# Kernel optimization log

Measured on AMD Instinct MI355X. Metric: run time of the kernel, lower is better.

Reference implementation:

```python
import jax, jax.numpy as jnp
import numpy as np

B, TQ, T, E, H, D = 4, 2048, 2048, 2048, 16, 128
BLOCK = 4096
THETA = 10000.0


def _rope_tables():
    # LlamaRotaryEmbedding cos/sin cache of length BLOCK
    inv_freq = 1.0 / (THETA ** (jnp.arange(0, D, 2, dtype=jnp.float32) / D))
    t = jnp.arange(BLOCK, dtype=jnp.float32)
    freqs = jnp.einsum('i,j->ij', t, inv_freq)          # [BLOCK, D/2]
    emb = jnp.concatenate([freqs, freqs], axis=-1)      # [BLOCK, D]
    return jnp.cos(emb), jnp.sin(emb)


def _rotate_half(x):
    x1, x2 = jnp.split(x, 2, axis=-1)
    return jnp.concatenate([-x2, x1], axis=-1)


def setup_inputs() -> dict:
    key = jax.random.key(0)
    ks = jax.random.split(key, 9)
    s = 0.02
    x = jax.random.normal(ks[0], (B, TQ, E), dtype=jnp.float32)
    xall = jax.random.normal(ks[1], (B, T, E), dtype=jnp.float32)
    posx = jnp.sort(jax.random.randint(ks[2], (B, TQ), 0, BLOCK), axis=-1)
    posxall = jnp.sort(jax.random.randint(ks[3], (B, T), 0, BLOCK), axis=-1)
    mask = jax.random.bernoulli(ks[4], 0.15, (B, T))  # True = masked out
    Wq = jax.random.normal(ks[5], (E, H * D), dtype=jnp.float32) * s
    Wk = jax.random.normal(ks[6], (E, H * D), dtype=jnp.float32) * s
    Wv = jax.random.normal(ks[7], (E, H * D), dtype=jnp.float32) * s
    Wo = jax.random.normal(ks[8], (H * D, E), dtype=jnp.float32) * s
    return {"x": x, "xall": xall, "posx": posx, "posxall": posxall,
            "mask": mask, "Wq": Wq, "Wk": Wk, "Wv": Wv, "Wo": Wo}


def reference(x, xall, posx, posxall, mask, Wq, Wk, Wv, Wo):
    cos, sin = _rope_tables()
    # projections -> [B, H, T, D]
    q = (x @ Wq).reshape(B, TQ, H, D).transpose(0, 2, 1, 3)
    k = (xall @ Wk).reshape(B, T, H, D).transpose(0, 2, 1, 3)
    v = (xall @ Wv).reshape(B, T, H, D).transpose(0, 2, 1, 3)
    # gather-based RoPE with arbitrary per-token positions
    cosq = cos[posx][:, None]      # [B,1,TQ,D]
    sinq = sin[posx][:, None]
    cosk = cos[posxall][:, None]   # [B,1,T,D]
    sink = sin[posxall][:, None]
    q = q * cosq + _rotate_half(q) * sinq
    k = k * cosk + _rotate_half(k) * sink
    # explicit O(T^2) attention
    att = jnp.einsum('bhqd,bhkd->bhqk', q, k) * (1.0 / np.sqrt(D))
    att = jnp.where(mask[:, None, None, :], jnp.finfo(att.dtype).min, att)
    att = jax.nn.softmax(att, axis=-1)
    y = jnp.einsum('bhqk,bhkd->bhqd', att, v)
    y = y.transpose(0, 2, 1, 3).reshape(B, TQ, H * D)
    return y @ Wo
```

## Files before the change

kernel.cpp:

```cpp
#include <hip/hip_runtime.h>

typedef __bf16 bf16x8 __attribute__((ext_vector_type(8)));
typedef float f32x4 __attribute__((ext_vector_type(4)));

#define B_ 4
#define H_ 16
#define T_ 2048
#define E_ 2048
#define D_ 128

#define GLDS(g, l)                                                   \
  __builtin_amdgcn_global_load_lds(                                  \
      (const __attribute__((address_space(1))) void*)(g),            \
      (__attribute__((address_space(3))) void*)(l), 16, 0, 0)

__global__ __launch_bounds__(256) void cvt_f32_bf16(const float* __restrict__ in,
                                                    __bf16* __restrict__ out) {
  size_t i = ((size_t)blockIdx.x * 256 + threadIdx.x) * 8;
  float4 a = *(const float4*)(in + i);
  float4 b = *(const float4*)(in + i + 4);
  bf16x8 v;
  v[0] = (__bf16)a.x; v[1] = (__bf16)a.y; v[2] = (__bf16)a.z; v[3] = (__bf16)a.w;
  v[4] = (__bf16)b.x; v[5] = (__bf16)b.y; v[6] = (__bf16)b.z; v[7] = (__bf16)b.w;
  *(bf16x8*)(out + i) = v;
}

__global__ __launch_bounds__(256) void transpose_w(const float* __restrict__ W,
                                                   __bf16* __restrict__ Wt) {
  __shared__ float tile[32][33];
  int bx = blockIdx.x & 63, by = blockIdx.x >> 6;
  int tx = threadIdx.x & 31, ty = threadIdx.x >> 5;
#pragma unroll
  for (int i = 0; i < 4; i++)
    tile[ty + i * 8][tx] = W[(size_t)(by * 32 + ty + i * 8) * 2048 + bx * 32 + tx];
  __syncthreads();
#pragma unroll
  for (int i = 0; i < 4; i++)
    Wt[(size_t)(bx * 32 + ty + i * 8) * 2048 + by * 32 + tx] =
        (__bf16)tile[tx][ty + i * 8];
}

template <typename TOut>
__global__ __launch_bounds__(256, 2)
void gemm_bt(const __bf16* __restrict__ A, const __bf16* __restrict__ Bt,
             TOut* __restrict__ C, int N, int K) {
  __shared__ alignas(16) __bf16 As[128 * 32];
  __shared__ alignas(16) __bf16 Bs[128 * 32];
  const int ntiles = N >> 7;
  const int tm = blockIdx.x / ntiles, tn = blockIdx.x % ntiles;
  const int tid = threadIdx.x;
  const int wave = tid >> 6, lane = tid & 63, quad = lane >> 4, l16 = lane & 15;
  const int wrow = (wave >> 1) << 6, wcol = (wave & 1) << 6;

  const f32x4 z4 = {0.f, 0.f, 0.f, 0.f};
  f32x4 acc[4][4];
#pragma unroll
  for (int r = 0; r < 4; r++)
#pragma unroll
    for (int c = 0; c < 4; c++) acc[r][c] = z4;

  const int srow = wave * 16 + (lane >> 2);
  const int skc = ((lane & 3) ^ ((lane >> 2) & 3)) << 3;
  const __bf16* gA = A + ((size_t)tm * 128 + srow) * K + skc;
  const __bf16* gB = Bt + ((size_t)tn * 128 + srow) * K + skc;
  __bf16* lA = &As[wave * 512];
  __bf16* lB = &Bs[wave * 512];

  for (int k0 = 0; k0 < K; k0 += 32) {
    __syncthreads();
    GLDS(gA + k0, lA);
    GLDS(gA + (size_t)64 * K + k0, lA + 2048);
    GLDS(gB + k0, lB);
    GLDS(gB + (size_t)64 * K + k0, lB + 2048);
    __syncthreads();

    bf16x8 af[4], bfr[4];
#pragma unroll
    for (int r = 0; r < 4; r++) {
      int ar = wrow + r * 16 + l16;
      af[r] = *(const bf16x8*)&As[ar * 32 + ((quad ^ (ar & 3)) << 3)];
    }
#pragma unroll
    for (int c = 0; c < 4; c++) {
      int br = wcol + c * 16 + l16;
      bfr[c] = *(const bf16x8*)&Bs[br * 32 + ((quad ^ (br & 3)) << 3)];
    }
#pragma unroll
    for (int r = 0; r < 4; r++)
#pragma unroll
      for (int c = 0; c < 4; c++)
        acc[r][c] =
            __builtin_amdgcn_mfma_f32_16x16x32_bf16(af[r], bfr[c], acc[r][c], 0, 0, 0);
  }

  const size_t rbase = (size_t)tm * 128 + wrow + quad * 4;
  const int cbase = tn * 128 + wcol + l16;
#pragma unroll
  for (int r = 0; r < 4; r++)
#pragma unroll
    for (int c = 0; c < 4; c++)
#pragma unroll
      for (int e = 0; e < 4; e++)
        C[(rbase + r * 16 + e) * N + cbase + c * 16] = (TOut)acc[r][c][e];
}

__global__ __launch_bounds__(256) void rope_relayout(const __bf16* __restrict__ raw,
                                                     const int* __restrict__ pos,
                                                     __bf16* __restrict__ out,
                                                     float scale) {
  int row = blockIdx.x;
  int b = row >> 11, t = row & 2047;
  float p = (float)pos[row];
  for (int i = threadIdx.x; i < 1024; i += 256) {
    int h = i >> 6, d = i & 63;
    float inv = exp2f((float)d * -0.2076205059304601f);
    float ang = p * inv;
    float c = cosf(ang) * scale, s = sinf(ang) * scale;
    float q1 = (float)raw[(size_t)row * 2048 + h * 128 + d];
    float q2 = (float)raw[(size_t)row * 2048 + h * 128 + d + 64];
    size_t o = ((size_t)(b * 16 + h) * 2048 + t) * 128 + d;
    out[o] = (__bf16)(q1 * c - q2 * s);
    out[o + 64] = (__bf16)(q2 * c + q1 * s);
  }
}

__global__ __launch_bounds__(256) void vtrans(const __bf16* __restrict__ Vraw,
                                              __bf16* __restrict__ Vt) {
  __shared__ __bf16 tile[32][33];
  int dt = blockIdx.x & 3, tt = (blockIdx.x >> 2) & 63, bh = blockIdx.x >> 8;
  int b = bh >> 4, h = bh & 15;
  int tx = threadIdx.x & 31, ty = threadIdx.x >> 5;
#pragma unroll
  for (int i = 0; i < 4; i++) {
    int t = tt * 32 + ty + i * 8;
    tile[ty + i * 8][tx] = Vraw[(size_t)(b * T_ + t) * 2048 + h * 128 + dt * 32 + tx];
  }
  __syncthreads();
#pragma unroll
  for (int i = 0; i < 4; i++) {
    int d = dt * 32 + ty + i * 8;
    Vt[((size_t)bh * 128 + d) * T_ + tt * 32 + tx] = tile[tx][ty + i * 8];
  }
}

__global__ __launch_bounds__(256, 2)
void attn(const __bf16* __restrict__ Q, const __bf16* __restrict__ K,
          const __bf16* __restrict__ Vt, const int* __restrict__ mask,
          __bf16* __restrict__ Y) {
  __shared__ alignas(16) __bf16 Ks[64][136];
  __shared__ alignas(16) __bf16 Vs[128][72];
  __shared__ alignas(16) __bf16 Ps[4][16][72];

  const int qt = blockIdx.x & 31;
  const int bh = blockIdx.x >> 5;
  const int b = bh >> 4;
  const __bf16* Qb = Q + (size_t)bh * T_ * 128;
  const __bf16* Kb = K + (size_t)bh * T_ * 128;
  const __bf16* Vb = Vt + (size_t)bh * 128 * T_;
  const int* mb = mask + (size_t)b * T_;

  const int tid = threadIdx.x, wave = tid >> 6, lane = tid & 63;
  const int quad = lane >> 4, l16 = lane & 15;

  bf16x8 qf[4];
  {
    int qrow = qt * 64 + wave * 16 + l16;
#pragma unroll
    for (int kc = 0; kc < 4; kc++)
      qf[kc] = *(const bf16x8*)(Qb + (size_t)qrow * 128 + kc * 32 + quad * 8);
  }

  const f32x4 z4 = {0.f, 0.f, 0.f, 0.f};
  f32x4 o[8];
#pragma unroll
  for (int n = 0; n < 8; n++) o[n] = z4;
  float lacc[4] = {0.f, 0.f, 0.f, 0.f};

  for (int t0 = 0; t0 < T_; t0 += 64) {
    __syncthreads();
#pragma unroll
    for (int rr = 0; rr < 4; rr++) {
      int idx = rr * 256 + tid;
      *(uint4*)&Ks[idx >> 4][(idx & 15) << 3] =
          *(const uint4*)(Kb + (size_t)(t0 + (idx >> 4)) * 128 + ((idx & 15) << 3));
      *(uint4*)&Vs[idx >> 3][(idx & 7) << 3] =
          *(const uint4*)(Vb + (size_t)(idx >> 3) * T_ + t0 + ((idx & 7) << 3));
    }
    __syncthreads();

    f32x4 s[4];
#pragma unroll
    for (int c = 0; c < 4; c++) s[c] = z4;
#pragma unroll
    for (int c = 0; c < 4; c++)
#pragma unroll
      for (int kc = 0; kc < 4; kc++) {
        bf16x8 kf = *(const bf16x8*)&Ks[c * 16 + l16][kc * 32 + quad * 8];
        s[c] = __builtin_amdgcn_mfma_f32_16x16x32_bf16(qf[kc], kf, s[c], 0, 0, 0);
      }

    int mk[4];
#pragma unroll
    for (int c = 0; c < 4; c++) mk[c] = mb[t0 + c * 16 + l16];

    float p[4][4];
#pragma unroll
    for (int c = 0; c < 4; c++)
#pragma unroll
      for (int e = 0; e < 4; e++) {
        float v = __builtin_amdgcn_exp2f(s[c][e]);
        p[c][e] = mk[c] ? 0.f : v;
      }
#pragma unroll
    for (int e = 0; e < 4; e++)
      lacc[e] += (p[0][e] + p[1][e]) + (p[2][e] + p[3][e]);

#pragma unroll
    for (int c = 0; c < 4; c++)
#pragma unroll
      for (int e = 0; e < 4; e++)
        Ps[wave][quad * 4 + e][c * 16 + l16] = (__bf16)p[c][e];
    __builtin_amdgcn_wave_barrier();

#pragma unroll
    for (int kc = 0; kc < 2; kc++) {
      bf16x8 pf = *(const bf16x8*)&Ps[wave][l16][kc * 32 + quad * 8];
#pragma unroll
      for (int n = 0; n < 8; n++) {
        bf16x8 vf = *(const bf16x8*)&Vs[n * 16 + l16][kc * 32 + quad * 8];
        o[n] = __builtin_amdgcn_mfma_f32_16x16x32_bf16(pf, vf, o[n], 0, 0, 0);
      }
    }
    __builtin_amdgcn_wave_barrier();
  }

  const int hcol = (bh & 15) * 128;
  const size_t yrow0 = (size_t)b * T_ + qt * 64 + wave * 16 + quad * 4;
#pragma unroll
  for (int e = 0; e < 4; e++) {
    float l = lacc[e];
    l += __shfl_xor(l, 1, 16);
    l += __shfl_xor(l, 2, 16);
    l += __shfl_xor(l, 4, 16);
    l += __shfl_xor(l, 8, 16);
    float inv = 1.f / l;
#pragma unroll
    for (int n = 0; n < 8; n++)
      Y[(yrow0 + e) * 2048 + hcol + n * 16 + l16] = (__bf16)(o[n][e] * inv);
  }
}

extern "C" void kernel_launch(void* const* d_in, const int* in_sizes, int n_in,
                              void* d_out, int out_size, void* d_ws, size_t ws_size,
                              hipStream_t stream) {
  const float* x = (const float*)d_in[0];
  const float* xall = (const float*)d_in[1];
  const int* posx = (const int*)d_in[2];
  const int* posxall = (const int*)d_in[3];
  const int* mask = (const int*)d_in[4];
  const float* Wq = (const float*)d_in[5];
  const float* Wk = (const float*)d_in[6];
  const float* Wv = (const float*)d_in[7];
  const float* Wo = (const float*)d_in[8];
  float* out = (float*)d_out;

  const size_t MB = 1024ull * 1024ull;
  if (ws_size < 192 * MB) return;
  char* ws = (char*)d_ws;
  __bf16* WqT   = (__bf16*)(ws + 0 * MB);
  __bf16* WkT   = (__bf16*)(ws + 8 * MB);
  __bf16* WvT   = (__bf16*)(ws + 16 * MB);
  __bf16* WoT   = (__bf16*)(ws + 24 * MB);
  __bf16* xb    = (__bf16*)(ws + 32 * MB);
  __bf16* xallb = (__bf16*)(ws + 64 * MB);
  __bf16* Qraw  = (__bf16*)(ws + 96 * MB);
  __bf16* Kraw  = (__bf16*)(ws + 128 * MB);
  __bf16* Vraw  = (__bf16*)(ws + 160 * MB);
  __bf16* Qr    = xb;
  __bf16* Kr    = xallb;
  __bf16* Vtp   = Qraw;
  __bf16* Y     = Kraw;

  const float QSCALE = (float)(0.08838834764831843 * 1.4426950408889634);

  cvt_f32_bf16<<<8192, 256, 0, stream>>>(x, xb);
  cvt_f32_bf16<<<8192, 256, 0, stream>>>(xall, xallb);

  transpose_w<<<4096, 256, 0, stream>>>(Wq, WqT);
  transpose_w<<<4096, 256, 0, stream>>>(Wk, WkT);
  transpose_w<<<4096, 256, 0, stream>>>(Wv, WvT);
  transpose_w<<<4096, 256, 0, stream>>>(Wo, WoT);

  gemm_bt<__bf16><<<1024, 256, 0, stream>>>(xb, WqT, Qraw, 2048, 2048);
  gemm_bt<__bf16><<<1024, 256, 0, stream>>>(xallb, WkT, Kraw, 2048, 2048);
  gemm_bt<__bf16><<<1024, 256, 0, stream>>>(xallb, WvT, Vraw, 2048, 2048);

  rope_relayout<<<8192, 256, 0, stream>>>(Qraw, posx, Qr, QSCALE);
  rope_relayout<<<8192, 256, 0, stream>>>(Kraw, posxall, Kr, 1.0f);
  vtrans<<<16384, 256, 0, stream>>>(Vraw, Vtp);

  attn<<<2048, 256, 0, stream>>>(Qr, Kr, Vtp, mask, Y);

  gemm_bt<float><<<1024, 256, 0, stream>>>(Y, WoT, out, 2048, 2048);
}
```

Measured before the change: 820.7 us.

## Double query rows per attention wave to reuse K/V tiles; swizzle P buffer

Each attention wave now processes 32 query rows (two 16-row sub-tiles) instead of 16, so each block covers 128 queries and the grid halves. Every K/V tile loaded into shared memory and every fragment read from LDS is reused for twice as many MFMAs, cutting global and LDS traffic per unit of work. The P staging buffer drops its padding and uses an XOR swizzle to avoid bank conflicts. The GEMM launch bound also goes to 3 blocks per CU. Register pressure rises in attention, and the smaller grid may reduce occupancy or load balance.

```diff
diff --git a/kernel.cpp b/kernel.cpp
--- a/kernel.cpp
+++ b/kernel.cpp
@@ -41,7 +41,7 @@
 }
 
 template <typename TOut>
-__global__ __launch_bounds__(256, 2)
+__global__ __launch_bounds__(256, 3)
 void gemm_bt(const __bf16* __restrict__ A, const __bf16* __restrict__ Bt,
              TOut* __restrict__ C, int N, int K) {
   __shared__ alignas(16) __bf16 As[128 * 32];
@@ -149,10 +149,10 @@
           __bf16* __restrict__ Y) {
   __shared__ alignas(16) __bf16 Ks[64][136];
   __shared__ alignas(16) __bf16 Vs[128][72];
-  __shared__ alignas(16) __bf16 Ps[4][16][72];
-
-  const int qt = blockIdx.x & 31;
-  const int bh = blockIdx.x >> 5;
+  __shared__ alignas(16) __bf16 Ps[4][32][64];
+
+  const int qt = blockIdx.x & 15;
+  const int bh = blockIdx.x >> 4;
   const int b = bh >> 4;
   const __bf16* Qb = Q + (size_t)bh * T_ * 128;
   const __bf16* Kb = K + (size_t)bh * T_ * 128;
@@ -162,19 +162,23 @@
   const int tid = threadIdx.x, wave = tid >> 6, lane = tid & 63;
   const int quad = lane >> 4, l16 = lane & 15;
 
-  bf16x8 qf[4];
+  bf16x8 qf[2][4];
   {
-    int qrow = qt * 64 + wave * 16 + l16;
-#pragma unroll
-    for (int kc = 0; kc < 4; kc++)
-      qf[kc] = *(const bf16x8*)(Qb + (size_t)qrow * 128 + kc * 32 + quad * 8);
+    int qrow = qt * 128 + wave * 32 + l16;
+#pragma unroll
+    for (int sub = 0; sub < 2; sub++)
+#pragma unroll
+      for (int kc = 0; kc < 4; kc++)
+        qf[sub][kc] =
+            *(const bf16x8*)(Qb + (size_t)(qrow + sub * 16) * 128 + kc * 32 + quad * 8);
   }
 
   const f32x4 z4 = {0.f, 0.f, 0.f, 0.f};
-  f32x4 o[8];
-#pragma unroll
-  for (int n = 0; n < 8; n++) o[n] = z4;
-  float lacc[4] = {0.f, 0.f, 0.f, 0.f};
+  f32x4 o0[8], o1[8];
+#pragma unroll
+  for (int n = 0; n < 8; n++) { o0[n] = z4; o1[n] = z4; }
+  float lacc0[4] = {0.f, 0.f, 0.f, 0.f};
+  float lacc1[4] = {0.f, 0.f, 0.f, 0.f};
 
   for (int t0 = 0; t0 < T_; t0 += 64) {
     __syncthreads();
@@ -188,65 +192,69 @@
     }
     __syncthreads();
 
-    f32x4 s[4];
-#pragma unroll
-    for (int c = 0; c < 4; c++) s[c] = z4;
+    f32x4 s0[4], s1[4];
+#pragma unroll
+    for (int c = 0; c < 4; c++) { s0[c] = z4; s1[c] = z4; }
 #pragma unroll
     for (int c = 0; c < 4; c++)
 #pragma unroll
       for (int kc = 0; kc < 4; kc++) {
         bf16x8 kf = *(const bf16x8*)&Ks[c * 16 + l16][kc * 32 + quad * 8];
-        s[c] = __builtin_amdgcn_mfma_f32_16x16x32_bf16(qf[kc], kf, s[c], 0, 0, 0);
+        s0[c] = __builtin_amdgcn_mfma_f32_16x16x32_bf16(qf[0][kc], kf, s0[c], 0, 0, 0);
+        s1[c] = __builtin_amdgcn_mfma_f32_16x16x32_bf16(qf[1][kc], kf, s1[c], 0, 0, 0);
       }
 
     int mk[4];
 #pragma unroll
     for (int c = 0; c < 4; c++) mk[c] = mb[t0 + c * 16 + l16];
 
-    float p[4][4];
-#pragma unroll
-    for (int c = 0; c < 4; c++)
+#pragma unroll
+    for (int c = 0; c < 4; c++) {
+      int pcol = (c * 16 + l16) ^ (quad << 4);
 #pragma unroll
       for (int e = 0; e < 4; e++) {
-        float v = __builtin_amdgcn_exp2f(s[c][e]);
-        p[c][e] = mk[c] ? 0.f : v;
+        float v0 = __builtin_amdgcn_exp2f(s0[c][e]);
+        float v1 = __builtin_amdgcn_exp2f(s1[c][e]);
+        v0 = mk[c] ? 0.f : v0;
+        v1 = mk[c] ? 0.f : v1;
+        lacc0[e] += v0;
+        lacc1[e] += v1;
+        Ps[wave][quad * 4 + e][pcol] = (__bf16)v0;
+        Ps[wave][16 + quad * 4 + e][pcol] = (__bf16)v1;
       }
-#pragma unroll
-    for (int e = 0; e < 4; e++)
-      lacc[e] += (p[0][e] + p[1][e]) + (p[2][e] + p[3][e]);
-
-#pragma unroll
-    for (int c = 0; c < 4; c++)
-#pragma unroll
-      for (int e = 0; e < 4; e++)
-        Ps[wave][quad * 4 + e][c * 16 + l16] = (__bf16)p[c][e];
+    }
     __builtin_amdgcn_wave_barrier();
 
+    const int g4 = (l16 >> 2) << 4;
 #pragma unroll
     for (int kc = 0; kc < 2; kc++) {
-      bf16x8 pf = *(const bf16x8*)&Ps[wave][l16][kc * 32 + quad * 8];
+      bf16x8 pf0 = *(const bf16x8*)&Ps[wave][l16][(kc * 32 + quad * 8) ^ g4];
+      bf16x8 pf1 = *(const bf16x8*)&Ps[wave][16 + l16][(kc * 32 + quad * 8) ^ g4];
 #pragma unroll
       for (int n = 0; n < 8; n++) {
         bf16x8 vf = *(const bf16x8*)&Vs[n * 16 + l16][kc * 32 + quad * 8];
-        o[n] = __builtin_amdgcn_mfma_f32_16x16x32_bf16(pf, vf, o[n], 0, 0, 0);
+        o0[n] = __builtin_amdgcn_mfma_f32_16x16x32_bf16(pf0, vf, o0[n], 0, 0, 0);
+        o1[n] = __builtin_amdgcn_mfma_f32_16x16x32_bf16(pf1, vf, o1[n], 0, 0, 0);
       }
     }
     __builtin_amdgcn_wave_barrier();
   }
 
   const int hcol = (bh & 15) * 128;
-  const size_t yrow0 = (size_t)b * T_ + qt * 64 + wave * 16 + quad * 4;
+  const size_t yrow0 = (size_t)b * T_ + qt * 128 + wave * 32 + quad * 4;
 #pragma unroll
   for (int e = 0; e < 4; e++) {
-    float l = lacc[e];
-    l += __shfl_xor(l, 1, 16);
-    l += __shfl_xor(l, 2, 16);
-    l += __shfl_xor(l, 4, 16);
-    l += __shfl_xor(l, 8, 16);
-    float inv = 1.f / l;
-#pragma unroll
-    for (int n = 0; n < 8; n++)
-      Y[(yrow0 + e) * 2048 + hcol + n * 16 + l16] = (__bf16)(o[n][e] * inv);
+    float l0 = lacc0[e], l1 = lacc1[e];
+    l0 += __shfl_xor(l0, 1, 16); l1 += __shfl_xor(l1, 1, 16);
+    l0 += __shfl_xor(l0, 2, 16); l1 += __shfl_xor(l1, 2, 16);
+    l0 += __shfl_xor(l0, 4, 16); l1 += __shfl_xor(l1, 4, 16);
+    l0 += __shfl_xor(l0, 8, 16); l1 += __shfl_xor(l1, 8, 16);
+    float i0 = 1.f / l0, i1 = 1.f / l1;
+#pragma unroll
+    for (int n = 0; n < 8; n++) {
+      Y[(yrow0 + e) * 2048 + hcol + n * 16 + l16] = (__bf16)(o0[n][e] * i0);
+      Y[(yrow0 + 16 + e) * 2048 + hcol + n * 16 + l16] = (__bf16)(o1[n][e] * i1);
+    }
   }
 }
 
@@ -299,7 +307,7 @@
   rope_relayout<<<8192, 256, 0, stream>>>(Kraw, posxall, Kr, 1.0f);
   vtrans<<<16384, 256, 0, stream>>>(Vraw, Vtp);
 
-  attn<<<2048, 256, 0, stream>>>(Qr, Kr, Vtp, mask, Y);
+  attn<<<1024, 256, 0, stream>>>(Qr, Kr, Vtp, mask, Y);
 
   gemm_bt<float><<<1024, 256, 0, stream>>>(Y, WoT, out, 2048, 2048);
 }
```

Result: faster. 764.7 us (-6.8%).
